# Optimization experiments

Measured on AMD Instinct MI355X. Metric: run time of the kernel, lower is better.

Reference implementation:

```python
import jax, jax.numpy as jnp
import numpy as np

B, S, D = 2, 2048, 768
C = 8                # num_channels
R = D // C           # ternary_rank = 96 (RoPE head_dim)
THETA = 10000.0
TERNARY_STD = 0.2
TERNARY_SCALE = 1.0  # ternary_factor_scaling


def _rope_tables():
    # HF-style RoPE: inv_freq over half dim, emb = concat(freqs, freqs)
    inv_freq = 1.0 / (THETA ** (np.arange(0, R, 2, dtype=np.float32) / R))
    pos = np.arange(S, dtype=np.float32)
    freqs = pos[:, None] * inv_freq[None, :]          # [S, R/2]
    emb = np.concatenate([freqs, freqs], axis=-1)     # [S, R]
    cos = np.broadcast_to(np.cos(emb)[None], (B, S, R)).copy()
    sin = np.broadcast_to(np.sin(emb)[None], (B, S, R)).copy()
    return jnp.asarray(cos), jnp.asarray(sin)


def setup_inputs() -> dict:
    key = jax.random.key(0)
    k1, k2, k3 = jax.random.split(key, 3)
    qz = jax.random.normal(k1, (B, S, D), dtype=jnp.float32)
    U = jax.random.normal(k2, (D, D), dtype=jnp.float32) * TERNARY_STD
    V = jax.random.normal(k3, (D, D), dtype=jnp.float32) * TERNARY_STD
    cos, sin = _rope_tables()
    return {"qz": qz, "cos": cos, "sin": sin, "U": U, "V": V}


def _rotate_half(x):
    h = x.shape[-1] // 2
    return jnp.concatenate([-x[..., h:], x[..., :h]], axis=-1)


def reference(qz, cos, sin, U, V):
    # cos/sin: [B,S,R] -> broadcast over channel dim -> [B,1,S,R]
    cosb = cos[:, None, :, :]
    sinb = sin[:, None, :, :]
    rope = lambda x: x * cosb + _rotate_half(x) * sinb       # apply
    rope_o = lambda x: x * cosb - _rotate_half(x) * sinb     # apply_o (inverse)

    # projections: F.linear(qz, W) == qz @ W.T
    qz_u = (qz @ U.T * TERNARY_SCALE).reshape(B, S, C, R).transpose(0, 2, 1, 3)
    qz_v = (qz @ V.T * TERNARY_SCALE).reshape(B, S, C, R).transpose(0, 2, 1, 3)

    qz_uo = rope_o(qz_u)
    qz_ur = rope(qz_u)
    qz_vr = rope(qz_v)

    # message_F: [B,C,S,S]
    message_F = jnp.einsum('bcqr,bckr->bcqk', qz_ur, qz_vr)
    # softmax(message_F / regularize_h) with regularize_h = 1/D  ->  * D
    qh = jax.nn.softmax((message_F * jnp.float32(D)).astype(jnp.float32), axis=-1).astype(qz_ur.dtype)

    qh_v1 = rope_o(jnp.einsum('bcqk,bckr->bcqr', qh, qz_vr))  # qh @ qz_v
    qh_v2 = rope(jnp.einsum('bckq,bckr->bcqr', qh, qz_uo))    # qh^T @ qz_uo

    qh_v1 = qh_v1.transpose(0, 2, 1, 3).reshape(B, S, D)
    qh_v2 = qh_v2.transpose(0, 2, 1, 3).reshape(B, S, D)

    message_G = (qh_v1 @ U + qh_v2 @ V) * TERNARY_SCALE
    return message_G
```

## Files before the change

### kernel.cpp

```cpp
#include <hip/hip_runtime.h>

typedef _Float16 f16;
typedef _Float16 f16x8 __attribute__((ext_vector_type(8)));
typedef _Float16 f16x4 __attribute__((ext_vector_type(4)));
typedef float f32x4 __attribute__((ext_vector_type(4)));

#define MFMA16(A,B,C) __builtin_amdgcn_mfma_f32_16x16x32_f16(A,B,C,0,0,0)
#define INV2048 4.8828125e-4f
#define HN (16ll*2048*96)
#define UVN 589824
#define ZC1 1107.98979f
#define ZC2 0.54101064f

__device__ __forceinline__ void split_f16(float x, f16& h, f16& l) {
    h = (f16)x;
    l = (f16)((x - (float)h) * 2048.0f);
}

__global__ __launch_bounds__(256) void k0_split(const float* __restrict__ qz,
                                                const float* __restrict__ U,
                                                const float* __restrict__ V,
                                                f16* __restrict__ qzh, f16* __restrict__ qzl,
                                                f16* __restrict__ Uh, f16* __restrict__ Ul,
                                                f16* __restrict__ Vh, f16* __restrict__ Vl) {
    const int i4 = blockIdx.x * 256 + threadIdx.x;
    {
        float4 x = *(const float4*)(qz + (size_t)i4 * 4);
        f16 h0, l0, h1, l1, h2, l2, h3, l3;
        split_f16(x.x, h0, l0); split_f16(x.y, h1, l1);
        split_f16(x.z, h2, l2); split_f16(x.w, h3, l3);
        f16x4 hv = {h0, h1, h2, h3};
        f16x4 lv = {l0, l1, l2, l3};
        *(f16x4*)(qzh + (size_t)i4 * 4) = hv;
        *(f16x4*)(qzl + (size_t)i4 * 4) = lv;
    }
    if (i4 < UVN / 4) {
        float4 x = *(const float4*)(U + (size_t)i4 * 4);
        f16 h0, l0, h1, l1, h2, l2, h3, l3;
        split_f16(x.x, h0, l0); split_f16(x.y, h1, l1);
        split_f16(x.z, h2, l2); split_f16(x.w, h3, l3);
        f16x4 hv = {h0, h1, h2, h3};
        f16x4 lv = {l0, l1, l2, l3};
        *(f16x4*)(Uh + (size_t)i4 * 4) = hv;
        *(f16x4*)(Ul + (size_t)i4 * 4) = lv;
        float4 y = *(const float4*)(V + (size_t)i4 * 4);
        split_f16(y.x, h0, l0); split_f16(y.y, h1, l1);
        split_f16(y.z, h2, l2); split_f16(y.w, h3, l3);
        f16x4 hv2 = {h0, h1, h2, h3};
        f16x4 lv2 = {l0, l1, l2, l3};
        *(f16x4*)(Vh + (size_t)i4 * 4) = hv2;
        *(f16x4*)(Vl + (size_t)i4 * 4) = lv2;
    }
}

__global__ __launch_bounds__(256, 2) void k1_proj(const f16* __restrict__ qzh,
                                                  const f16* __restrict__ qzl,
                                                  const f16* __restrict__ Uh,
                                                  const f16* __restrict__ Ul,
                                                  const f16* __restrict__ Vh,
                                                  const f16* __restrict__ Vl,
                                                  const float* __restrict__ cosb,
                                                  const float* __restrict__ sinb,
                                                  f16* __restrict__ uhp, f16* __restrict__ ulp,
                                                  f16* __restrict__ vhp, f16* __restrict__ vlp,
                                                  f16* __restrict__ vT, f16* __restrict__ oT) {
    __shared__ __align__(16) f16 smem[36864];
    f16* sAh  = smem;
    f16* sAl  = smem + 4608;
    f16* sBuh = smem + 9216;
    f16* sBul = smem + 9216 + 6912;
    f16* sBvh = smem + 9216 + 2 * 6912;
    f16* sBvl = smem + 9216 + 3 * 6912;

    const int tid = threadIdx.x;
    const int w = tid >> 6, lane = tid & 63;
    const int quad = lane >> 4, l15 = lane & 15;
    const int wr = w >> 1, wc = w & 1;
    const int bs0 = blockIdx.x * 64;
    const int c = blockIdx.y;

    const f16* Ug_h = Uh + (size_t)c * 96 * 768;
    const f16* Ug_l = Ul + (size_t)c * 96 * 768;
    const f16* Vg_h = Vh + (size_t)c * 96 * 768;
    const f16* Vg_l = Vl + (size_t)c * 96 * 768;

    f32x4 aUS[2][3] = {}, aUX[2][3] = {};
    f32x4 aVS[2][3] = {}, aVX[2][3] = {};

    for (int k0 = 0; k0 < 768; k0 += 64) {
        __syncthreads();
#pragma unroll
        for (int m = 0; m < 2; ++m) {
            int f = tid + 256 * m, row = f >> 3, cg = f & 7;
            const size_t go = (size_t)(bs0 + row) * 768 + k0 + cg * 8;
            const int lo = row * 72 + cg * 8;
            *(float4*)&sAh[lo] = *(const float4*)(qzh + go);
            *(float4*)&sAl[lo] = *(const float4*)(qzl + go);
        }
#pragma unroll
        for (int m = 0; m < 3; ++m) {
            int f = tid + 256 * m, row = f >> 3, cg = f & 7;
            const size_t go = (size_t)row * 768 + k0 + cg * 8;
            const int lo = row * 72 + cg * 8;
            *(float4*)&sBuh[lo] = *(const float4*)(Ug_h + go);
            *(float4*)&sBul[lo] = *(const float4*)(Ug_l + go);
            *(float4*)&sBvh[lo] = *(const float4*)(Vg_h + go);
            *(float4*)&sBvl[lo] = *(const float4*)(Vg_l + go);
        }
        __syncthreads();
#pragma unroll
        for (int cc = 0; cc < 2; ++cc) {
            f16x8 ah[2], al[2];
#pragma unroll
            for (int mt = 0; mt < 2; ++mt) {
                const int ar = (32 * wr + 16 * mt + l15) * 72 + cc * 32 + quad * 8;
                ah[mt] = *(const f16x8*)&sAh[ar];
                al[mt] = *(const f16x8*)&sAl[ar];
            }
#pragma unroll
            for (int nt = 0; nt < 3; ++nt) {
                const int br = (48 * wc + 16 * nt + l15) * 72 + cc * 32 + quad * 8;
                f16x8 buh = *(const f16x8*)&sBuh[br];
                f16x8 bul = *(const f16x8*)&sBul[br];
                f16x8 bvh = *(const f16x8*)&sBvh[br];
                f16x8 bvl = *(const f16x8*)&sBvl[br];
#pragma unroll
                for (int mt = 0; mt < 2; ++mt) {
                    aUS[mt][nt] = MFMA16(ah[mt], buh, aUS[mt][nt]);
                    aUX[mt][nt] = MFMA16(ah[mt], bul, aUX[mt][nt]);
                    aUX[mt][nt] = MFMA16(al[mt], buh, aUX[mt][nt]);
                    aVS[mt][nt] = MFMA16(ah[mt], bvh, aVS[mt][nt]);
                    aVX[mt][nt] = MFMA16(ah[mt], bvl, aVX[mt][nt]);
                    aVX[mt][nt] = MFMA16(al[mt], bvh, aVX[mt][nt]);
                }
            }
        }
    }

    __syncthreads();
    float* LU = (float*)smem;
    float* LV = LU + 6400;
#pragma unroll
    for (int mt = 0; mt < 2; ++mt)
#pragma unroll
        for (int nt = 0; nt < 3; ++nt)
#pragma unroll
            for (int r = 0; r < 4; ++r) {
                const int sl = 32 * wr + 16 * mt + 4 * quad + r;
                const int col = 48 * wc + 16 * nt + l15;
                LU[sl * 100 + col] = aUS[mt][nt][r] + aUX[mt][nt][r] * INV2048;
                LV[sl * 100 + col] = aVS[mt][nt][r] + aVX[mt][nt][r] * INV2048;
            }
    __syncthreads();

    const int b = bs0 >> 11;
    const int s0 = bs0 & 2047;
    const int head = b * 8 + c;
    const size_t nb = (size_t)head * 2048 * 96;
    const size_t tb = (size_t)head * 96 * 2048;
    const int ty = tid >> 4, tx = tid & 15;

#pragma unroll
    for (int jj = 0; jj < 3; ++jj) {
        int r = tx + 16 * jj;
        f16 vt1[4], vt2[4], ot1[4], ot2[4];
#pragma unroll
        for (int ii = 0; ii < 4; ++ii) {
            int sl = 4 * ty + ii;
            int s = s0 + sl;
            int cbi = (b * 2048 + s) * 96 + r;
            float cc = cosb[cbi], ss = sinb[cbi];
            size_t rowb = nb + (size_t)s * 96;
            float u1 = LU[sl * 100 + r], u2 = LU[sl * 100 + r + 48];
            float v1 = LV[sl * 100 + r], v2 = LV[sl * 100 + r + 48];
            float ur1 = u1 * cc - u2 * ss, ur2 = u2 * cc + u1 * ss;
            float uo1 = u1 * cc + u2 * ss, uo2 = u2 * cc - u1 * ss;
            float vr1 = v1 * cc - v2 * ss, vr2 = v2 * cc + v1 * ss;
            f16 h, l;
            split_f16(ur1, h, l); uhp[rowb + r] = h;      ulp[rowb + r] = l;
            split_f16(ur2, h, l); uhp[rowb + r + 48] = h; ulp[rowb + r + 48] = l;
            split_f16(vr1, h, l); vhp[rowb + r] = h;      vlp[rowb + r] = l;      vt1[ii] = h;
            split_f16(vr2, h, l); vhp[rowb + r + 48] = h; vlp[rowb + r + 48] = l; vt2[ii] = h;
            ot1[ii] = (f16)uo1; ot2[ii] = (f16)uo2;
        }
        f16x4 pv1 = {vt1[0], vt1[1], vt1[2], vt1[3]};
        f16x4 pv2 = {vt2[0], vt2[1], vt2[2], vt2[3]};
        f16x4 po1 = {ot1[0], ot1[1], ot1[2], ot1[3]};
        f16x4 po2 = {ot2[0], ot2[1], ot2[2], ot2[3]};
        *(f16x4*)&vT[tb + (size_t)r * 2048 + s0 + 4 * ty] = pv1;
        *(f16x4*)&vT[tb + (size_t)(r + 48) * 2048 + s0 + 4 * ty] = pv2;
        *(f16x4*)&oT[tb + (size_t)r * 2048 + s0 + 4 * ty] = po1;
        *(f16x4*)&oT[tb + (size_t)(r + 48) * 2048 + s0 + 4 * ty] = po2;
    }
}

__global__ __launch_bounds__(256, 2) void k2_stats(const f16* __restrict__ uhp,
                                                   const f16* __restrict__ ulp,
                                                   const f16* __restrict__ vhp,
                                                   const f16* __restrict__ vlp,
                                                   float* __restrict__ Mo) {
    __shared__ f16 Bh[2][64 * 104];
    __shared__ f16 Bl[2][64 * 104];
    __shared__ float Mbuf[4][64];
    const int tid = threadIdx.x, w = tid >> 6, lane = tid & 63;
    const int quad = lane >> 4, l15 = lane & 15;
    const int q0 = blockIdx.x * 64, head = blockIdx.y;
    const f16* Ah_g = uhp + (size_t)head * 2048 * 96;
    const f16* Al_g = ulp + (size_t)head * 2048 * 96;
    const f16* Bh_g = vhp + (size_t)head * 2048 * 96;
    const f16* Bl_g = vlp + (size_t)head * 2048 * 96;

    f16x8 Afh[4][3], Afl[4][3];
#pragma unroll
    for (int mt = 0; mt < 4; ++mt)
#pragma unroll
        for (int cc = 0; cc < 3; ++cc) {
            size_t off = (size_t)(q0 + 16 * mt + l15) * 96 + cc * 32 + quad * 8;
            Afh[mt][cc] = *(const f16x8*)(Ah_g + off);
            Afl[mt][cc] = *(const f16x8*)(Al_g + off);
        }

    const int sr0 = tid / 12,         sc0 = (tid % 12) * 8;
    const int sr1 = (tid + 256) / 12, sc1 = ((tid + 256) % 12) * 8;
    const int sr2 = (tid + 512) / 12, sc2 = ((tid + 512) % 12) * 8;

    float4 h0, h1, h2, g0, g1, g2;

    float m_run[4][4];
#pragma unroll
    for (int mt = 0; mt < 4; ++mt)
#pragma unroll
        for (int r = 0; r < 4; ++r) m_run[mt][r] = -3.0e38f;

    h0 = *(const float4*)(Bh_g + (size_t)sr0 * 96 + sc0);
    h1 = *(const float4*)(Bh_g + (size_t)sr1 * 96 + sc1);
    h2 = *(const float4*)(Bh_g + (size_t)sr2 * 96 + sc2);
    g0 = *(const float4*)(Bl_g + (size_t)sr0 * 96 + sc0);
    g1 = *(const float4*)(Bl_g + (size_t)sr1 * 96 + sc1);
    g2 = *(const float4*)(Bl_g + (size_t)sr2 * 96 + sc2);
    *(float4*)&Bh[0][sr0 * 104 + sc0] = h0;
    *(float4*)&Bh[0][sr1 * 104 + sc1] = h1;
    *(float4*)&Bh[0][sr2 * 104 + sc2] = h2;
    *(float4*)&Bl[0][sr0 * 104 + sc0] = g0;
    *(float4*)&Bl[0][sr1 * 104 + sc1] = g1;
    *(float4*)&Bl[0][sr2 * 104 + sc2] = g2;
    __syncthreads();

    for (int t = 0; t < 32; ++t) {
        const int cur = t & 1;
        if (t < 31) {
            const f16* bg = Bh_g + (size_t)(t + 1) * 6144;
            const f16* lg = Bl_g + (size_t)(t + 1) * 6144;
            h0 = *(const float4*)(bg + (size_t)sr0 * 96 + sc0);
            h1 = *(const float4*)(bg + (size_t)sr1 * 96 + sc1);
            h2 = *(const float4*)(bg + (size_t)sr2 * 96 + sc2);
            g0 = *(const float4*)(lg + (size_t)sr0 * 96 + sc0);
            g1 = *(const float4*)(lg + (size_t)sr1 * 96 + sc1);
            g2 = *(const float4*)(lg + (size_t)sr2 * 96 + sc2);
        }
        f32x4 accS[4] = {}, accX[4] = {};
#pragma unroll
        for (int cc = 0; cc < 3; ++cc) {
            f16x8 bh = *(const f16x8*)&Bh[cur][(w * 16 + l15) * 104 + cc * 32 + quad * 8];
            f16x8 bl = *(const f16x8*)&Bl[cur][(w * 16 + l15) * 104 + cc * 32 + quad * 8];
#pragma unroll
            for (int mt = 0; mt < 4; ++mt) {
                accS[mt] = MFMA16(Afh[mt][cc], bh, accS[mt]);
                accX[mt] = MFMA16(Afh[mt][cc], bl, accX[mt]);
                accX[mt] = MFMA16(Afl[mt][cc], bh, accX[mt]);
            }
        }
#pragma unroll
        for (int mt = 0; mt < 4; ++mt)
#pragma unroll
            for (int r = 0; r < 4; ++r) {
                float zl = fmaf(ZC1, accS[mt][r], ZC2 * accX[mt][r]);
                m_run[mt][r] = fmaxf(m_run[mt][r], zl);
            }
        if (t < 31) {
            *(float4*)&Bh[cur ^ 1][sr0 * 104 + sc0] = h0;
            *(float4*)&Bh[cur ^ 1][sr1 * 104 + sc1] = h1;
            *(float4*)&Bh[cur ^ 1][sr2 * 104 + sc2] = h2;
            *(float4*)&Bl[cur ^ 1][sr0 * 104 + sc0] = g0;
            *(float4*)&Bl[cur ^ 1][sr1 * 104 + sc1] = g1;
            *(float4*)&Bl[cur ^ 1][sr2 * 104 + sc2] = g2;
        }
        __syncthreads();
    }
#pragma unroll
    for (int mt = 0; mt < 4; ++mt)
#pragma unroll
        for (int r = 0; r < 4; ++r) {
            float m = m_run[mt][r];
            m = fmaxf(m, __shfl_xor(m, 1)); m = fmaxf(m, __shfl_xor(m, 2));
            m = fmaxf(m, __shfl_xor(m, 4)); m = fmaxf(m, __shfl_xor(m, 8));
            m_run[mt][r] = m;
        }
    if (l15 == 0) {
#pragma unroll
        for (int mt = 0; mt < 4; ++mt)
#pragma unroll
            for (int r = 0; r < 4; ++r)
                Mbuf[w][16 * mt + 4 * quad + r] = m_run[mt][r];
    }
    __syncthreads();
    if (tid < 64) {
        float M = -3.0e38f;
#pragma unroll
        for (int ww = 0; ww < 4; ++ww) M = fmaxf(M, Mbuf[ww][tid]);
        Mo[head * 2048 + q0 + tid] = M;
    }
}

__global__ __launch_bounds__(256, 2) void k3a(const f16* __restrict__ uhp,
                                              const f16* __restrict__ ulp,
                                              const f16* __restrict__ vhp,
                                              const f16* __restrict__ vlp,
                                              const f16* __restrict__ vT,
                                              const float* __restrict__ Mo,
                                              float* __restrict__ Lo,
                                              const float* __restrict__ cosb,
                                              const float* __restrict__ sinb,
                                              f16* __restrict__ w1) {
    __shared__ f16 Bh[64 * 104];
    __shared__ f16 Bl[64 * 104];
    __shared__ f16 Vt[2][112 * 72];
    __shared__ f16 P[64 * 72];
    const int tid = threadIdx.x, w = tid >> 6, lane = tid & 63;
    const int quad = lane >> 4, l15 = lane & 15;
    const int q0 = blockIdx.x * 64, head = blockIdx.y;
    const f16* Ah_g = uhp + (size_t)head * 2048 * 96;
    const f16* Al_g = ulp + (size_t)head * 2048 * 96;
    const f16* Bh_g = vhp + (size_t)head * 2048 * 96;
    const f16* Bl_g = vlp + (size_t)head * 2048 * 96;
    const f16* Vt_g = vT + (size_t)head * 96 * 2048;

    f16x8 Afh[4][3], Afl[4][3];
#pragma unroll
    for (int mt = 0; mt < 4; ++mt)
#pragma unroll
        for (int cc = 0; cc < 3; ++cc) {
            size_t off = (size_t)(q0 + 16 * mt + l15) * 96 + cc * 32 + quad * 8;
            Afh[mt][cc] = *(const f16x8*)(Ah_g + off);
            Afl[mt][cc] = *(const f16x8*)(Al_g + off);
        }
    float negM[4][4];
#pragma unroll
    for (int mt = 0; mt < 4; ++mt)
#pragma unroll
        for (int r = 0; r < 4; ++r)
            negM[mt][r] = -Mo[head * 2048 + q0 + 16 * mt + 4 * quad + r];

    const int sr0 = tid / 12,         sc0 = (tid % 12) * 8;
    const int sr1 = (tid + 256) / 12, sc1 = ((tid + 256) % 12) * 8;
    const int sr2 = (tid + 512) / 12, sc2 = ((tid + 512) % 12) * 8;
    const int vr0 = tid >> 3, vcc = (tid & 7) * 8;

    float4 h0, h1, h2, g0, g1, g2, v0, v1, v2;

    if (tid < 144) {
        f16x8 ones = {(f16)1, (f16)1, (f16)1, (f16)1,
                      (f16)1, (f16)1, (f16)1, (f16)1};
        *(f16x8*)&Vt[0][96 * 72 + tid * 8] = ones;
        *(f16x8*)&Vt[1][96 * 72 + tid * 8] = ones;
    }

    h0 = *(const float4*)(Bh_g + (size_t)sr0 * 96 + sc0);
    h1 = *(const float4*)(Bh_g + (size_t)sr1 * 96 + sc1);
    h2 = *(const float4*)(Bh_g + (size_t)sr2 * 96 + sc2);
    g0 = *(const float4*)(Bl_g + (size_t)sr0 * 96 + sc0);
    g1 = *(const float4*)(Bl_g + (size_t)sr1 * 96 + sc1);
    g2 = *(const float4*)(Bl_g + (size_t)sr2 * 96 + sc2);
    v0 = *(const float4*)(Vt_g + (size_t)vr0 * 2048 + vcc);
    v1 = *(const float4*)(Vt_g + (size_t)(vr0 + 32) * 2048 + vcc);
    v2 = *(const float4*)(Vt_g + (size_t)(vr0 + 64) * 2048 + vcc);
    *(float4*)&Bh[sr0 * 104 + sc0] = h0;
    *(float4*)&Bh[sr1 * 104 + sc1] = h1;
    *(float4*)&Bh[sr2 * 104 + sc2] = h2;
    *(float4*)&Bl[sr0 * 104 + sc0] = g0;
    *(float4*)&Bl[sr1 * 104 + sc1] = g1;
    *(float4*)&Bl[sr2 * 104 + sc2] = g2;
    *(float4*)&Vt[0][vr0 * 72 + vcc] = v0;
    *(float4*)&Vt[0][(vr0 + 32) * 72 + vcc] = v1;
    *(float4*)&Vt[0][(vr0 + 64) * 72 + vcc] = v2;
    __syncthreads();

    f32x4 accO[7] = {};
    int pcur = 0;

    for (int t = 0; t < 32; ++t) {
        if (t < 31) {
            const f16* bg = Bh_g + (size_t)(t + 1) * 6144;
            const f16* lg = Bl_g + (size_t)(t + 1) * 6144;
            const int kn = (t + 1) * 64;
            h0 = *(const float4*)(bg + (size_t)sr0 * 96 + sc0);
            h1 = *(const float4*)(bg + (size_t)sr1 * 96 + sc1);
            h2 = *(const float4*)(bg + (size_t)sr2 * 96 + sc2);
            g0 = *(const float4*)(lg + (size_t)sr0 * 96 + sc0);
            g1 = *(const float4*)(lg + (size_t)sr1 * 96 + sc1);
            g2 = *(const float4*)(lg + (size_t)sr2 * 96 + sc2);
            v0 = *(const float4*)(Vt_g + (size_t)vr0 * 2048 + kn + vcc);
            v1 = *(const float4*)(Vt_g + (size_t)(vr0 + 32) * 2048 + kn + vcc);
            v2 = *(const float4*)(Vt_g + (size_t)(vr0 + 64) * 2048 + kn + vcc);
        }
        f32x4 accS[4] = {}, accX[4] = {};
#pragma unroll
        for (int cc = 0; cc < 3; ++cc) {
            f16x8 bh = *(const f16x8*)&Bh[(w * 16 + l15) * 104 + cc * 32 + quad * 8];
            f16x8 bl = *(const f16x8*)&Bl[(w * 16 + l15) * 104 + cc * 32 + quad * 8];
#pragma unroll
            for (int mt = 0; mt < 4; ++mt) {
                accS[mt] = MFMA16(Afh[mt][cc], bh, accS[mt]);
                accX[mt] = MFMA16(Afh[mt][cc], bl, accX[mt]);
                accX[mt] = MFMA16(Afl[mt][cc], bh, accX[mt]);
            }
        }
#pragma unroll
        for (int mt = 0; mt < 4; ++mt)
#pragma unroll
            for (int r = 0; r < 4; ++r) {
                float zl = fmaf(ZC1, accS[mt][r], ZC2 * accX[mt][r]);
                P[(16 * mt + 4 * quad + r) * 72 + w * 16 + l15] =
                    (f16)exp2f(zl + negM[mt][r]);
            }
        __syncthreads();
        if (t < 31) {
            *(float4*)&Bh[sr0 * 104 + sc0] = h0;
            *(float4*)&Bh[sr1 * 104 + sc1] = h1;
            *(float4*)&Bh[sr2 * 104 + sc2] = h2;
            *(float4*)&Bl[sr0 * 104 + sc0] = g0;
            *(float4*)&Bl[sr1 * 104 + sc1] = g1;
            *(float4*)&Bl[sr2 * 104 + sc2] = g2;
            *(float4*)&Vt[pcur ^ 1][vr0 * 72 + vcc] = v0;
            *(float4*)&Vt[pcur ^ 1][(vr0 + 32) * 72 + vcc] = v1;
            *(float4*)&Vt[pcur ^ 1][(vr0 + 64) * 72 + vcc] = v2;
        }
#pragma unroll
        for (int kc = 0; kc < 2; ++kc) {
            f16x8 ap = *(const f16x8*)&P[(w * 16 + l15) * 72 + kc * 32 + quad * 8];
#pragma unroll
            for (int nt = 0; nt < 7; ++nt) {
                f16x8 bv = *(const f16x8*)&Vt[pcur][(nt * 16 + l15) * 72 + kc * 32 + quad * 8];
                accO[nt] = MFMA16(ap, bv, accO[nt]);
            }
        }
        __syncthreads();
        pcur ^= 1;
    }
    float invL[4];
#pragma unroll
    for (int r = 0; r < 4; ++r) invL[r] = 1.0f / accO[6][r];
    if (l15 == 0) {
#pragma unroll
        for (int r = 0; r < 4; ++r)
            Lo[head * 2048 + q0 + w * 16 + quad * 4 + r] = accO[6][r];
    }

    const int b = head >> 3, c = head & 7;
#pragma unroll
    for (int r = 0; r < 4; ++r) {
        int q = q0 + w * 16 + quad * 4 + r;
        int cbi = (b * 2048 + q) * 96;
        f16* wrow = w1 + (size_t)(b * 2048 + q) * 768 + c * 96;
#pragma unroll
        for (int nt = 0; nt < 3; ++nt) {
            int rr = nt * 16 + l15;
            float cc = cosb[cbi + rr], ss = sinb[cbi + rr];
            float a = accO[nt][r] * invL[r];
            float b2 = accO[nt + 3][r] * invL[r];
            wrow[rr] = (f16)(a * cc + b2 * ss);
            wrow[rr + 48] = (f16)(b2 * cc - a * ss);
        }
    }
}

__global__ __launch_bounds__(256, 2) void k3b(const f16* __restrict__ uhp,
                                              const f16* __restrict__ ulp,
                                              const f16* __restrict__ vhp,
                                              const f16* __restrict__ vlp,
                                              const f16* __restrict__ oT,
                                              const float* __restrict__ Mo,
                                              const float* __restrict__ Lo,
                                              const float* __restrict__ cosb,
                                              const float* __restrict__ sinb,
                                              f16* __restrict__ w2) {
    __shared__ f16 Bh[64 * 104];
    __shared__ f16 Bl[64 * 104];
    __shared__ f16 Ot[2][96 * 72];
    __shared__ f16 P[64 * 72];
    const int tid = threadIdx.x, w = tid >> 6, lane = tid & 63;
    const int quad = lane >> 4, l15 = lane & 15;
    const int q0 = blockIdx.x * 64, head = blockIdx.y;
    const f16* Ah_g = vhp + (size_t)head * 2048 * 96;
    const f16* Al_g = vlp + (size_t)head * 2048 * 96;
    const f16* Bh_g = uhp + (size_t)head * 2048 * 96;
    const f16* Bl_g = ulp + (size_t)head * 2048 * 96;
    const f16* Ot_g = oT + (size_t)head * 96 * 2048;

    f16x8 Afh[4][3], Afl[4][3];
#pragma unroll
    for (int mt = 0; mt < 4; ++mt)
#pragma unroll
        for (int cc = 0; cc < 3; ++cc) {
            size_t off = (size_t)(q0 + 16 * mt + l15) * 96 + cc * 32 + quad * 8;
            Afh[mt][cc] = *(const f16x8*)(Ah_g + off);
            Afl[mt][cc] = *(const f16x8*)(Al_g + off);
        }

    const int sr0 = tid / 12,         sc0 = (tid % 12) * 8;
    const int sr1 = (tid + 256) / 12, sc1 = ((tid + 256) % 12) * 8;
    const int sr2 = (tid + 512) / 12, sc2 = ((tid + 512) % 12) * 8;
    const int vr0 = tid >> 3, vcc = (tid & 7) * 8;

    float4 h0, h1, h2, g0, g1, g2, v0, v1, v2;

    h0 = *(const float4*)(Bh_g + (size_t)sr0 * 96 + sc0);
    h1 = *(const float4*)(Bh_g + (size_t)sr1 * 96 + sc1);
    h2 = *(const float4*)(Bh_g + (size_t)sr2 * 96 + sc2);
    g0 = *(const float4*)(Bl_g + (size_t)sr0 * 96 + sc0);
    g1 = *(const float4*)(Bl_g + (size_t)sr1 * 96 + sc1);
    g2 = *(const float4*)(Bl_g + (size_t)sr2 * 96 + sc2);
    v0 = *(const float4*)(Ot_g + (size_t)vr0 * 2048 + vcc);
    v1 = *(const float4*)(Ot_g + (size_t)(vr0 + 32) * 2048 + vcc);
    v2 = *(const float4*)(Ot_g + (size_t)(vr0 + 64) * 2048 + vcc);
    *(float4*)&Bh[sr0 * 104 + sc0] = h0;
    *(float4*)&Bh[sr1 * 104 + sc1] = h1;
    *(float4*)&Bh[sr2 * 104 + sc2] = h2;
    *(float4*)&Bl[sr0 * 104 + sc0] = g0;
    *(float4*)&Bl[sr1 * 104 + sc1] = g1;
    *(float4*)&Bl[sr2 * 104 + sc2] = g2;
    *(float4*)&Ot[0][vr0 * 72 + vcc] = v0;
    *(float4*)&Ot[0][(vr0 + 32) * 72 + vcc] = v1;
    *(float4*)&Ot[0][(vr0 + 64) * 72 + vcc] = v2;
    __syncthreads();

    f32x4 accO[6] = {};
    int pcur = 0;

    for (int t = 0; t < 32; ++t) {
        const int k0 = t * 64;
        float negMk = -Mo[head * 2048 + k0 + w * 16 + l15];
        float invLk = 1.0f / Lo[head * 2048 + k0 + w * 16 + l15];
        if (t < 31) {
            const f16* bg = Bh_g + (size_t)(t + 1) * 6144;
            const f16* lg = Bl_g + (size_t)(t + 1) * 6144;
            const int kn = (t + 1) * 64;
            h0 = *(const float4*)(bg + (size_t)sr0 * 96 + sc0);
            h1 = *(const float4*)(bg + (size_t)sr1 * 96 + sc1);
            h2 = *(const float4*)(bg + (size_t)sr2 * 96 + sc2);
            g0 = *(const float4*)(lg + (size_t)sr0 * 96 + sc0);
            g1 = *(const float4*)(lg + (size_t)sr1 * 96 + sc1);
            g2 = *(const float4*)(lg + (size_t)sr2 * 96 + sc2);
            v0 = *(const float4*)(Ot_g + (size_t)vr0 * 2048 + kn + vcc);
            v1 = *(const float4*)(Ot_g + (size_t)(vr0 + 32) * 2048 + kn + vcc);
            v2 = *(const float4*)(Ot_g + (size_t)(vr0 + 64) * 2048 + kn + vcc);
        }
        f32x4 accS[4] = {}, accX[4] = {};
#pragma unroll
        for (int cc = 0; cc < 3; ++cc) {
            f16x8 bh = *(const f16x8*)&Bh[(w * 16 + l15) * 104 + cc * 32 + quad * 8];
            f16x8 bl = *(const f16x8*)&Bl[(w * 16 + l15) * 104 + cc * 32 + quad * 8];
#pragma unroll
            for (int mt = 0; mt < 4; ++mt) {
                accS[mt] = MFMA16(Afh[mt][cc], bh, accS[mt]);
                accX[mt] = MFMA16(Afl[mt][cc], bh, accX[mt]);
                accX[mt] = MFMA16(Afh[mt][cc], bl, accX[mt]);
            }
        }
#pragma unroll
        for (int mt = 0; mt < 4; ++mt)
#pragma unroll
            for (int r = 0; r < 4; ++r) {
                float zl = fmaf(ZC1, accS[mt][r], ZC2 * accX[mt][r]);
                P[(16 * mt + 4 * quad + r) * 72 + w * 16 + l15] =
                    (f16)(exp2f(zl + negMk) * invLk);
            }
        __syncthreads();
        if (t < 31) {
            *(float4*)&Bh[sr0 * 104 + sc0] = h0;
            *(float4*)&Bh[sr1 * 104 + sc1] = h1;
            *(float4*)&Bh[sr2 * 104 + sc2] = h2;
            *(float4*)&Bl[sr0 * 104 + sc0] = g0;
            *(float4*)&Bl[sr1 * 104 + sc1] = g1;
            *(float4*)&Bl[sr2 * 104 + sc2] = g2;
            *(float4*)&Ot[pcur ^ 1][vr0 * 72 + vcc] = v0;
            *(float4*)&Ot[pcur ^ 1][(vr0 + 32) * 72 + vcc] = v1;
            *(float4*)&Ot[pcur ^ 1][(vr0 + 64) * 72 + vcc] = v2;
        }
#pragma unroll
        for (int kc = 0; kc < 2; ++kc) {
            f16x8 ap = *(const f16x8*)&P[(w * 16 + l15) * 72 + kc * 32 + quad * 8];
#pragma unroll
            for (int nt = 0; nt < 6; ++nt) {
                f16x8 bo = *(const f16x8*)&Ot[pcur][(nt * 16 + l15) * 72 + kc * 32 + quad * 8];
                accO[nt] = MFMA16(ap, bo, accO[nt]);
            }
        }
        __syncthreads();
        pcur ^= 1;
    }
    const int b = head >> 3, c = head & 7;
#pragma unroll
    for (int r = 0; r < 4; ++r) {
        int q = q0 + w * 16 + quad * 4 + r;
        int cbi = (b * 2048 + q) * 96;
        f16* wrow = w2 + (size_t)(b * 2048 + q) * 768 + c * 96;
#pragma unroll
        for (int nt = 0; nt < 3; ++nt) {
            int rr = nt * 16 + l15;
            float cc = cosb[cbi + rr], ss = sinb[cbi + rr];
            float a = accO[nt][r];
            float b2 = accO[nt + 3][r];
            wrow[rr] = (f16)(a * cc - b2 * ss);
            wrow[rr + 48] = (f16)(b2 * cc + a * ss);
        }
    }
}

__global__ __launch_bounds__(256, 2) void k4_final(const f16* __restrict__ w1,
                                                   const f16* __restrict__ w2,
                                                   const float* __restrict__ U,
                                                   const float* __restrict__ V,
                                                   float* __restrict__ outp) {
    __shared__ f16 A1[128 * 56];
    __shared__ f16 A2[128 * 56];
    __shared__ f16 B1[64 * 56];
    __shared__ f16 B2[64 * 56];
    const int tid = threadIdx.x, w = tid >> 6, lane = tid & 63;
    const int quad = lane >> 4, l15 = lane & 15;
    const int bs0 = blockIdx.x * 128;
    const int d0 = blockIdx.y * 64;
    f32x4 acc[2][4] = {};

    for (int ec = 0; ec < 24; ++ec) {
        int e0 = ec * 32;
        __syncthreads();
#pragma unroll
        for (int m = 0; m < 2; ++m) {
            int f = tid + 256 * m;
            int row = f >> 2, q = f & 3;
            *(float4*)&A1[row * 56 + q * 8] =
                *(const float4*)(w1 + (size_t)(bs0 + row) * 768 + e0 + q * 8);
            *(float4*)&A2[row * 56 + q * 8] =
                *(const float4*)(w2 + (size_t)(bs0 + row) * 768 + e0 + q * 8);
        }
#pragma unroll
        for (int m2 = 0; m2 < 2; ++m2) {
            int e_r = (tid >> 4) + 16 * m2;
            int dc = tid & 15;
            float4 fu = *(const float4*)(U + (size_t)(e0 + e_r) * 768 + d0 + dc * 4);
            float4 fv = *(const float4*)(V + (size_t)(e0 + e_r) * 768 + d0 + dc * 4);
            B1[(dc * 4 + 0) * 56 + e_r] = (f16)fu.x;
            B1[(dc * 4 + 1) * 56 + e_r] = (f16)fu.y;
            B1[(dc * 4 + 2) * 56 + e_r] = (f16)fu.z;
            B1[(dc * 4 + 3) * 56 + e_r] = (f16)fu.w;
            B2[(dc * 4 + 0) * 56 + e_r] = (f16)fv.x;
            B2[(dc * 4 + 1) * 56 + e_r] = (f16)fv.y;
            B2[(dc * 4 + 2) * 56 + e_r] = (f16)fv.z;
            B2[(dc * 4 + 3) * 56 + e_r] = (f16)fv.w;
        }
        __syncthreads();
        f16x8 a1f[2], a2f[2];
#pragma unroll
        for (int mt = 0; mt < 2; ++mt) {
            a1f[mt] = *(const f16x8*)&A1[(32 * w + 16 * mt + l15) * 56 + quad * 8];
            a2f[mt] = *(const f16x8*)&A2[(32 * w + 16 * mt + l15) * 56 + quad * 8];
        }
#pragma unroll
        for (int nt = 0; nt < 4; ++nt) {
            f16x8 b1f = *(const f16x8*)&B1[(nt * 16 + l15) * 56 + quad * 8];
            f16x8 b2f = *(const f16x8*)&B2[(nt * 16 + l15) * 56 + quad * 8];
#pragma unroll
            for (int mt = 0; mt < 2; ++mt) {
                acc[mt][nt] = MFMA16(a1f[mt], b1f, acc[mt][nt]);
                acc[mt][nt] = MFMA16(a2f[mt], b2f, acc[mt][nt]);
            }
        }
    }
#pragma unroll
    for (int mt = 0; mt < 2; ++mt)
#pragma unroll
        for (int nt = 0; nt < 4; ++nt)
#pragma unroll
            for (int r = 0; r < 4; ++r) {
                int s = bs0 + 32 * w + 16 * mt + 4 * quad + r;
                int d = d0 + 16 * nt + l15;
                outp[(size_t)s * 768 + d] = acc[mt][nt][r];
            }
}

extern "C" void kernel_launch(void* const* d_in, const int* in_sizes, int n_in,
                              void* d_out, int out_size, void* d_ws, size_t ws_size,
                              hipStream_t stream) {
    const float* qz   = (const float*)d_in[0];
    const float* cosb = (const float*)d_in[1];
    const float* sinb = (const float*)d_in[2];
    const float* U    = (const float*)d_in[3];
    const float* V    = (const float*)d_in[4];
    float* outp = (float*)d_out;

    f16* ws16 = (f16*)d_ws;
    f16* uhp = ws16;
    f16* ulp = ws16 + HN;
    f16* vhp = ws16 + 2 * HN;
    f16* vlp = ws16 + 3 * HN;
    f16* vT  = ws16 + 4 * HN;
    f16* oT  = ws16 + 5 * HN;
    f16* w1  = ws16 + 6 * HN;
    f16* w2  = ws16 + 7 * HN;
    float* Mo = (float*)(ws16 + 8 * HN);
    float* Lo = Mo + 16 * 2048;

    f16* qzh = w1;
    f16* qzl = w2;
    f16* outw = (f16*)d_out;
    f16* Uh = outw;
    f16* Ul = outw + UVN;
    f16* Vh = outw + 2 * UVN;
    f16* Vl = outw + 3 * UVN;

    k0_split<<<dim3(3072), 256, 0, stream>>>(qz, U, V, qzh, qzl, Uh, Ul, Vh, Vl);
    k1_proj<<<dim3(64, 8), 256, 0, stream>>>(qzh, qzl, Uh, Ul, Vh, Vl, cosb, sinb,
                                             uhp, ulp, vhp, vlp, vT, oT);
    k2_stats<<<dim3(32, 16), 256, 0, stream>>>(uhp, ulp, vhp, vlp, Mo);
    k3a<<<dim3(32, 16), 256, 0, stream>>>(uhp, ulp, vhp, vlp, vT, Mo, Lo, cosb, sinb, w1);
    k3b<<<dim3(32, 16), 256, 0, stream>>>(uhp, ulp, vhp, vlp, oT, Mo, Lo, cosb, sinb, w2);
    k4_final<<<dim3(32, 12), 256, 0, stream>>>(w1, w2, U, V, outp);
}
```

Baseline: 334.3 us.

## Swizzle block order, add MFMA priority hints, and XOR-swizzle P tile in LDS

Remaps block indices so that consecutive workgroups are spread across heads and channels, which is meant to improve L2/XCD locality. Raises wave priority with s_setprio around the MFMA loops so matrix work is favoured over other waves. XOR-swizzles the P staging tile writes and reads to cut LDS bank conflicts. The swizzle must stay consistent between the write and read patterns, and the block remap assumes the grid has exactly 512 blocks.

New measurement: 333.2 us. About the same (-0.3%).

```diff
diff --git a/kernel.cpp b/kernel.cpp
--- a/kernel.cpp
+++ b/kernel.cpp
@@ -76,8 +76,10 @@
     const int w = tid >> 6, lane = tid & 63;
     const int quad = lane >> 4, l15 = lane & 15;
     const int wr = w >> 1, wc = w & 1;
-    const int bs0 = blockIdx.x * 64;
-    const int c = blockIdx.y;
+    const int bid0 = blockIdx.y * 64 + blockIdx.x;
+    const int swz  = (bid0 & 7) * 64 + (bid0 >> 3);
+    const int bs0 = (swz & 63) * 64;
+    const int c = swz >> 6;
 
     const f16* Ug_h = Uh + (size_t)c * 96 * 768;
     const f16* Ug_l = Ul + (size_t)c * 96 * 768;
@@ -204,7 +206,9 @@
     __shared__ float Mbuf[4][64];
     const int tid = threadIdx.x, w = tid >> 6, lane = tid & 63;
     const int quad = lane >> 4, l15 = lane & 15;
-    const int q0 = blockIdx.x * 64, head = blockIdx.y;
+    const int bid0 = blockIdx.y * 32 + blockIdx.x;
+    const int swz  = (bid0 & 7) * 64 + (bid0 >> 3);
+    const int q0 = (swz & 31) * 64, head = swz >> 5;
     const f16* Ah_g = uhp + (size_t)head * 2048 * 96;
     const f16* Al_g = ulp + (size_t)head * 2048 * 96;
     const f16* Bh_g = vhp + (size_t)head * 2048 * 96;
@@ -259,6 +263,7 @@
             g2 = *(const float4*)(lg + (size_t)sr2 * 96 + sc2);
         }
         f32x4 accS[4] = {}, accX[4] = {};
+        __builtin_amdgcn_s_setprio(1);
 #pragma unroll
         for (int cc = 0; cc < 3; ++cc) {
             f16x8 bh = *(const f16x8*)&Bh[cur][(w * 16 + l15) * 104 + cc * 32 + quad * 8];
@@ -270,6 +275,7 @@
                 accX[mt] = MFMA16(Afl[mt][cc], bh, accX[mt]);
             }
         }
+        __builtin_amdgcn_s_setprio(0);
 #pragma unroll
         for (int mt = 0; mt < 4; ++mt)
 #pragma unroll
@@ -328,7 +334,9 @@
     __shared__ f16 P[64 * 72];
     const int tid = threadIdx.x, w = tid >> 6, lane = tid & 63;
     const int quad = lane >> 4, l15 = lane & 15;
-    const int q0 = blockIdx.x * 64, head = blockIdx.y;
+    const int bid0 = blockIdx.y * 32 + blockIdx.x;
+    const int swz  = (bid0 & 7) * 64 + (bid0 >> 3);
+    const int q0 = (swz & 31) * 64, head = swz >> 5;
     const f16* Ah_g = uhp + (size_t)head * 2048 * 96;
     const f16* Al_g = ulp + (size_t)head * 2048 * 96;
     const f16* Bh_g = vhp + (size_t)head * 2048 * 96;
@@ -355,6 +363,9 @@
     const int sr1 = (tid + 256) / 12, sc1 = ((tid + 256) % 12) * 8;
     const int sr2 = (tid + 512) / 12, sc2 = ((tid + 512) % 12) * 8;
     const int vr0 = tid >> 3, vcc = (tid & 7) * 8;
+
+    const int pwsw = (quad & 2) << 4;
+    const int prsw = (l15 & 8) << 2;
 
     float4 h0, h1, h2, g0, g1, g2, v0, v1, v2;
 
@@ -404,6 +415,7 @@
             v2 = *(const float4*)(Vt_g + (size_t)(vr0 + 64) * 2048 + kn + vcc);
         }
         f32x4 accS[4] = {}, accX[4] = {};
+        __builtin_amdgcn_s_setprio(1);
 #pragma unroll
         for (int cc = 0; cc < 3; ++cc) {
             f16x8 bh = *(const f16x8*)&Bh[(w * 16 + l15) * 104 + cc * 32 + quad * 8];
@@ -415,12 +427,13 @@
                 accX[mt] = MFMA16(Afl[mt][cc], bh, accX[mt]);
             }
         }
+        __builtin_amdgcn_s_setprio(0);
 #pragma unroll
         for (int mt = 0; mt < 4; ++mt)
 #pragma unroll
             for (int r = 0; r < 4; ++r) {
                 float zl = fmaf(ZC1, accS[mt][r], ZC2 * accX[mt][r]);
-                P[(16 * mt + 4 * quad + r) * 72 + w * 16 + l15] =
+                P[(16 * mt + 4 * quad + r) * 72 + ((w * 16 + l15) ^ pwsw)] =
                     (f16)exp2f(zl + negM[mt][r]);
             }
         __syncthreads();
@@ -435,15 +448,18 @@
             *(float4*)&Vt[pcur ^ 1][(vr0 + 32) * 72 + vcc] = v1;
             *(float4*)&Vt[pcur ^ 1][(vr0 + 64) * 72 + vcc] = v2;
         }
+        __builtin_amdgcn_s_setprio(1);
 #pragma unroll
         for (int kc = 0; kc < 2; ++kc) {
-            f16x8 ap = *(const f16x8*)&P[(w * 16 + l15) * 72 + kc * 32 + quad * 8];
+            f16x8 ap = *(const f16x8*)&P[(w * 16 + l15) * 72 +
+                                         ((kc * 32 + quad * 8) ^ prsw)];
 #pragma unroll
             for (int nt = 0; nt < 7; ++nt) {
                 f16x8 bv = *(const f16x8*)&Vt[pcur][(nt * 16 + l15) * 72 + kc * 32 + quad * 8];
                 accO[nt] = MFMA16(ap, bv, accO[nt]);
             }
         }
+        __builtin_amdgcn_s_setprio(0);
         __syncthreads();
         pcur ^= 1;
     }
@@ -490,7 +506,9 @@
     __shared__ f16 P[64 * 72];
     const int tid = threadIdx.x, w = tid >> 6, lane = tid & 63;
     const int quad = lane >> 4, l15 = lane & 15;
-    const int q0 = blockIdx.x * 64, head = blockIdx.y;
+    const int bid0 = blockIdx.y * 32 + blockIdx.x;
+    const int swz  = (bid0 & 7) * 64 + (bid0 >> 3);
+    const int q0 = (swz & 31) * 64, head = swz >> 5;
     const f16* Ah_g = vhp + (size_t)head * 2048 * 96;
     const f16* Al_g = vlp + (size_t)head * 2048 * 96;
     const f16* Bh_g = uhp + (size_t)head * 2048 * 96;
@@ -511,6 +529,9 @@
     const int sr1 = (tid + 256) / 12, sc1 = ((tid + 256) % 12) * 8;
     const int sr2 = (tid + 512) / 12, sc2 = ((tid + 512) % 12) * 8;
     const int vr0 = tid >> 3, vcc = (tid & 7) * 8;
+
+    const int pwsw = (quad & 2) << 4;
+    const int prsw = (l15 & 8) << 2;
 
     float4 h0, h1, h2, g0, g1, g2, v0, v1, v2;
 
@@ -556,6 +577,7 @@
             v2 = *(const float4*)(Ot_g + (size_t)(vr0 + 64) * 2048 + kn + vcc);
         }
         f32x4 accS[4] = {}, accX[4] = {};
+        __builtin_amdgcn_s_setprio(1);
 #pragma unroll
         for (int cc = 0; cc < 3; ++cc) {
             f16x8 bh = *(const f16x8*)&Bh[(w * 16 + l15) * 104 + cc * 32 + quad * 8];
@@ -567,12 +589,13 @@
                 accX[mt] = MFMA16(Afh[mt][cc], bl, accX[mt]);
             }
         }
+        __builtin_amdgcn_s_setprio(0);
 #pragma unroll
         for (int mt = 0; mt < 4; ++mt)
 #pragma unroll
             for (int r = 0; r < 4; ++r) {
                 float zl = fmaf(ZC1, accS[mt][r], ZC2 * accX[mt][r]);
-                P[(16 * mt + 4 * quad + r) * 72 + w * 16 + l15] =
+                P[(16 * mt + 4 * quad + r) * 72 + ((w * 16 + l15) ^ pwsw)] =
                     (f16)(exp2f(zl + negMk) * invLk);
             }
         __syncthreads();
@@ -587,15 +610,18 @@
             *(float4*)&Ot[pcur ^ 1][(vr0 + 32) * 72 + vcc] = v1;
             *(float4*)&Ot[pcur ^ 1][(vr0 + 64) * 72 + vcc] = v2;
         }
+        __builtin_amdgcn_s_setprio(1);
 #pragma unroll
         for (int kc = 0; kc < 2; ++kc) {
-            f16x8 ap = *(const f16x8*)&P[(w * 16 + l15) * 72 + kc * 32 + quad * 8];
+            f16x8 ap = *(const f16x8*)&P[(w * 16 + l15) * 72 +
+                                         ((kc * 32 + quad * 8) ^ prsw)];
 #pragma unroll
             for (int nt = 0; nt < 6; ++nt) {
                 f16x8 bo = *(const f16x8*)&Ot[pcur][(nt * 16 + l15) * 72 + kc * 32 + quad * 8];
                 accO[nt] = MFMA16(ap, bo, accO[nt]);
             }
         }
+        __builtin_amdgcn_s_setprio(0);
         __syncthreads();
         pcur ^= 1;
     }
```
